# Optimization experiments

Measured on AMD Instinct MI355X. Metric: run time of the kernel, lower is better.

Reference implementation:

```python
import jax, jax.numpy as jnp
import numpy as np

IMG = 1024       # original image resolution implied by (1024 - 1) normalization
STRIDE = 16
TEMP = 0.1
EPS = 1e-12      # F.normalize eps


def setup_inputs() -> dict:
    key = jax.random.key(0)
    k1, k2, k3, k4, k5 = jax.random.split(key, 5)
    B, C, Hf, Wf, N = 32, 256, 64, 64, 128
    feats_src = jax.random.normal(k1, (B, C, Hf, Wf), dtype=jnp.float32)
    feats_trg = jax.random.normal(k2, (B, C, Hf, Wf), dtype=jnp.float32)
    kps_src = jax.random.uniform(k3, (B, N, 2), dtype=jnp.float32) * (IMG - 1)
    kps_trg = jax.random.uniform(k4, (B, N, 2), dtype=jnp.float32) * (IMG - 1)
    kps_mask = jax.random.randint(k5, (B, N), 0, 2, dtype=jnp.int32)
    return {"feats_src": feats_src, "feats_trg": feats_trg,
            "kps_src": kps_src, "kps_trg": kps_trg, "kps_mask": kps_mask}


def _l2norm_c(x):
    # F.normalize(x, dim=1): x / max(||x||_2, eps) along channel dim
    n = jnp.sqrt(jnp.sum(x * x, axis=1, keepdims=True))
    return x / jnp.maximum(n, EPS)


def _bilinear_sample(feats, kps):
    # feats: [B,C,Hf,Wf]; kps: [B,N,2] pixel coords in [0, IMG-1]
    # Equivalent to F.grid_sample(align_corners=True, bilinear) with
    # grid = kps/(IMG-1)*2-1 -> pixel coords kps/(IMG-1)*(size-1).
    B, C, Hf, Wf = feats.shape
    x = kps[..., 0] / (IMG - 1) * (Wf - 1)  # [B,N]
    y = kps[..., 1] / (IMG - 1) * (Hf - 1)
    x0 = jnp.clip(jnp.floor(x), 0, Wf - 1).astype(jnp.int32)
    y0 = jnp.clip(jnp.floor(y), 0, Hf - 1).astype(jnp.int32)
    x1 = jnp.clip(x0 + 1, 0, Wf - 1)
    y1 = jnp.clip(y0 + 1, 0, Hf - 1)
    fx = x - x0.astype(x.dtype)
    fy = y - y0.astype(y.dtype)
    ft = jnp.transpose(feats, (0, 2, 3, 1))      # [B,Hf,Wf,C]
    bb = jnp.arange(B)[:, None]                  # [B,1] broadcasts to [B,N]
    g = lambda yy, xx: ft[bb, yy, xx]            # [B,N,C]
    wa = ((1 - fx) * (1 - fy))[..., None]
    wb = ((1 - fx) * fy)[..., None]
    wc = (fx * (1 - fy))[..., None]
    wd = (fx * fy)[..., None]
    return wa * g(y0, x0) + wb * g(y1, x0) + wc * g(y0, x1) + wd * g(y1, x1)


def reference(feats_src, feats_trg, kps_src, kps_trg, kps_mask):
    B, C, Hf, Wf = feats_src.shape
    N = kps_src.shape[1]
    fs = _l2norm_c(feats_src)
    ftg = _l2norm_c(feats_trg)

    # Query features sampled at source keypoints: [B,N,C]
    q = _bilinear_sample(fs, kps_src)

    # Logits over all target spatial positions: [B,N,Hf*Wf]
    trg_flat = ftg.reshape(B, C, Hf * Wf)
    logits = jnp.einsum('bnc,bcm->bnm', q, trg_flat) / TEMP

    # Bilinear soft targets at target keypoints (feature-grid coords)
    gx = kps_trg[..., 0] / STRIDE
    gy = kps_trg[..., 1] / STRIDE
    x0 = jnp.clip(jnp.floor(gx), 0, Wf - 1).astype(jnp.int32)
    x1 = jnp.clip(x0 + 1, 0, Wf - 1)
    y0 = jnp.clip(jnp.floor(gy), 0, Hf - 1).astype(jnp.int32)
    y1 = jnp.clip(y0 + 1, 0, Hf - 1)
    x0f, x1f = x0.astype(gx.dtype), x1.astype(gx.dtype)
    y0f, y1f = y0.astype(gy.dtype), y1.astype(gy.dtype)
    wa = (x1f - gx) * (y1f - gy)
    wb = (x1f - gx) * (gy - y0f)
    wc = (gx - x0f) * (y1f - gy)
    wd = (gx - x0f) * (gy - y0f)

    m = (kps_mask != 0).astype(logits.dtype)     # [B,N]
    w = jnp.stack([wa, wb, wc, wd], axis=-1) * m[..., None]   # [B,N,4]
    idx = jnp.stack([y0 * Wf + x0, y1 * Wf + x0,
                     y0 * Wf + x1, y1 * Wf + x1], axis=-1)    # [B,N,4]
    bb = jnp.arange(B)[:, None, None]
    nn = jnp.arange(N)[None, :, None]
    soft_targets = jnp.zeros_like(logits).at[bb, nn, idx].add(w)

    log_probs = jax.nn.log_softmax(logits, axis=-1)
    loss = -(soft_targets * log_probs).sum(axis=-1)           # [B,N]
    denom = jnp.maximum(m.sum(), 1.0)
    return (loss * m).sum() / denom
```

## Files before the change

### kernel.cpp

```cpp
#include <hip/hip_runtime.h>
#include <math.h>

#define B_    32
#define C_    256
#define HF    64
#define WF    64
#define M_    4096
#define N_    128
#define IMGM1 1023.0f
#define TEMP_ 0.1f
#define EPS_  1e-12f
#define NCH   32
#define SAS   40

typedef __attribute__((ext_vector_type(8))) short short8;
typedef __attribute__((ext_vector_type(4))) float floatx4;

__device__ __forceinline__ unsigned short f2bf(float x) {
  unsigned int u = __float_as_uint(x);
  u += 0x7fffu + ((u >> 16) & 1u);
  return (unsigned short)(u >> 16);
}
__device__ __forceinline__ float bf2f(unsigned short h) {
  return __uint_as_float(((unsigned int)h) << 16);
}
__device__ __forceinline__ float wave_sum(float v) {
#pragma unroll
  for (int off = 32; off; off >>= 1) v += __shfl_down(v, off, 64);
  return v;
}

__device__ __forceinline__ void src_geom(float kx, float ky, int& x0, int& y0,
                                         int& x1, int& y1, float& fx, float& fy) {
  const float x = kx / IMGM1 * (float)(WF - 1);
  const float y = ky / IMGM1 * (float)(HF - 1);
  x0 = (int)fminf(fmaxf(floorf(x), 0.f), 63.f);
  y0 = (int)fminf(fmaxf(floorf(y), 0.f), 63.f);
  x1 = min(x0 + 1, 63);
  y1 = min(y0 + 1, 63);
  fx = x - (float)x0;
  fy = y - (float)y0;
}

__global__ __launch_bounds__(256) void k1a_stage(const float* __restrict__ fs,
                                                 const float* __restrict__ kps,
                                                 ushort* __restrict__ corner,
                                                 float* __restrict__ ssqg) {
  const int cg = blockIdx.x, b = blockIdx.y, t = threadIdx.x;
  const int c0 = cg * 2;
  __shared__ __align__(16) float plane[2 * M_];
  __shared__ float4 ssq2[256];

  const float4* src = (const float4*)(fs + ((size_t)(b * C_ + c0)) * M_);
  float4* dst = (float4*)plane;
#pragma unroll
  for (int i = 0; i < 8; i++) dst[t + 256 * i] = src[t + 256 * i];
  __syncthreads();

  const int n = t & 127, p = t >> 7;
  const int c = c0 + p;
  const float kx = kps[((size_t)b * N_ + n) * 2 + 0];
  const float ky = kps[((size_t)b * N_ + n) * 2 + 1];
  int x0, y0, x1, y1; float fx, fy;
  src_geom(kx, ky, x0, y0, x1, y1, fx, fy);

  const float* pl = plane + p * M_;
  const float f00 = pl[y0 * WF + x0];
  const float f10 = pl[y1 * WF + x0];
  const float f01 = pl[y0 * WF + x1];
  const float f11 = pl[y1 * WF + x1];

  ushort4 cr;
  cr.x = f2bf(f00); cr.y = f2bf(f10); cr.z = f2bf(f01); cr.w = f2bf(f11);
  *(ushort4*)&corner[(((size_t)b * C_ + c) * N_ + n) * 4] = cr;

  ssq2[t] = make_float4(f00 * f00, f10 * f10, f01 * f01, f11 * f11);
  __syncthreads();
  if (t < 128) {
    const float4 a = ssq2[t], bq = ssq2[t + 128];
    float* g = ssqg + ((size_t)b * N_ + t) * 4;
    atomicAdd(g + 0, a.x + bq.x);
    atomicAdd(g + 1, a.y + bq.y);
    atomicAdd(g + 2, a.z + bq.z);
    atomicAdd(g + 3, a.w + bq.w);
  }
}

__global__ __launch_bounds__(256) void k1b2_combine(const ushort* __restrict__ corner,
                                                    const float* __restrict__ ssqg,
                                                    const float* __restrict__ kps,
                                                    ushort* __restrict__ qbf) {
  const int cg = blockIdx.x, b = blockIdx.y, t = threadIdx.x;
  __shared__ float4 uw[128];
  __shared__ ushort sQ[32][137];

  if (t < 128) {
    const int n = t;
    const float kx = kps[((size_t)b * N_ + n) * 2 + 0];
    const float ky = kps[((size_t)b * N_ + n) * 2 + 1];
    int x0, y0, x1, y1; float fx, fy;
    src_geom(kx, ky, x0, y0, x1, y1, fx, fy);
    const float wa = (1.f - fx) * (1.f - fy), wb = (1.f - fx) * fy;
    const float wc = fx * (1.f - fy), wd = fx * fy;
    const float4 sq = *(const float4*)&ssqg[((size_t)b * N_ + n) * 4];
    const float r0 = 1.f / fmaxf(sqrtf(sq.x), EPS_);
    const float r1 = 1.f / fmaxf(sqrtf(sq.y), EPS_);
    const float r2 = 1.f / fmaxf(sqrtf(sq.z), EPS_);
    const float r3 = 1.f / fmaxf(sqrtf(sq.w), EPS_);
    uw[n] = make_float4(wa * r0, wb * r1, wc * r2, wd * r3);
  }
  __syncthreads();

  const ushort* cb = corner + (((size_t)b * C_ + cg * 32) * N_) * 4;
#pragma unroll
  for (int i = 0; i < 16; i++) {
    const int e = t + 256 * i;
    const int n = e & 127, cl = e >> 7;
    const ushort4 cr = *(const ushort4*)&cb[((size_t)cl * N_ + n) * 4];
    const float4 u = uw[n];
    const float qv = u.x * bf2f(cr.x) + u.y * bf2f(cr.y) +
                     u.z * bf2f(cr.z) + u.w * bf2f(cr.w);
    sQ[cl][n] = f2bf(qv);
  }
  __syncthreads();

  ushort* qb = qbf + (size_t)b * N_ * C_ + cg * 32;
#pragma unroll
  for (int i = 0; i < 4; i++) {
    const int o = t + 256 * i;
    const int n = o >> 3, c4 = (o & 7) * 4;
    ushort4 w4;
    w4.x = sQ[c4 + 0][n]; w4.y = sQ[c4 + 1][n];
    w4.z = sQ[c4 + 2][n]; w4.w = sQ[c4 + 3][n];
    *(ushort4*)&qb[(size_t)n * C_ + c4] = w4;
  }
}

__global__ __launch_bounds__(256, 4) void k2_mfma(const float* __restrict__ trg,
                                                  const ushort* __restrict__ qbf,
                                                  const float* __restrict__ kps_trg,
                                                  const int* __restrict__ mask,
                                                  float2* __restrict__ part,
                                                  float* __restrict__ tacc) {
  const int t = threadIdx.x;
  const int mb = blockIdx.x, b = blockIdx.y;
  const int m0 = mb * 128;
  const int wave = t >> 6, lane = t & 63;
  const int wn = wave >> 1, wm = wave & 1;
  const int lg = lane >> 4, ln = lane & 15;

  __shared__ __align__(16) short sA[128 * SAS];
  __shared__ __align__(16) short sB[128 * SAS];
  __shared__ __align__(16) float ssqp[16 * 128];
  __shared__ float scl[128];
  __shared__ float2 lser[128 * 2];
  __shared__ __align__(16) int   tidx[128][4];
  __shared__ __align__(16) float tw[128][4];
  __shared__ unsigned tmask[128];

  floatx4 acc[4][4];
#pragma unroll
  for (int i = 0; i < 4; i++)
#pragma unroll
    for (int j = 0; j < 4; j++) acc[i][j] = (floatx4)0.f;

  float ssq[8];
#pragma unroll
  for (int e = 0; e < 8; e++) ssq[e] = 0.f;

  const ushort* qb = qbf + (size_t)b * N_ * C_;
  const float*  tb = trg + (size_t)b * C_ * M_ + m0;
  const int kk  = 2 * (t >> 4);
  const int m4  = (t & 15) * 4;
  const int gB  = kk >> 3;
  const int kin = kk & 7;

  const ushort* qA0 = qb + (t >> 2) * C_ + (t & 3) * 8;
  const ushort* qA1 = qA0 + 64 * C_;
  const int aoff = (t >> 2) * SAS + (t & 3) * 8;
  const float* tbase = tb + (size_t)kk * M_ + m4;

  short8 rA0, rA1;
  float4 rBa0, rBa1, rBb0, rBb1;

  rA0 = *(const short8*)(qA0);
  rA1 = *(const short8*)(qA1);
  {
    const float* p0 = tbase;
    const float* p1 = p0 + M_;
    rBa0 = *(const float4*)p0;  rBa1 = *(const float4*)(p0 + 64);
    rBb0 = *(const float4*)p1;  rBb1 = *(const float4*)(p1 + 64);
  }

  for (int k0 = 0; k0 < C_; k0 += 32) {
    *(short8*)&sA[aoff] = rA0;
    *(short8*)&sA[aoff + 64 * SAS] = rA1;
    {
      const float v0[8] = {rBa0.x, rBa0.y, rBa0.z, rBa0.w, rBa1.x, rBa1.y, rBa1.z, rBa1.w};
      const float v1[8] = {rBb0.x, rBb0.y, rBb0.z, rBb0.w, rBb1.x, rBb1.y, rBb1.z, rBb1.w};
#pragma unroll
      for (int e = 0; e < 8; e++) {
        ssq[e] += v0[e] * v0[e] + v1[e] * v1[e];
        const int m = m4 + (e & 3) + ((e >> 2) << 6);
        const int fm = (m >> 3) & 3;
        const unsigned int pr = (unsigned int)f2bf(v0[e]) | ((unsigned int)f2bf(v1[e]) << 16);
        *(unsigned int*)&sB[m * SAS + ((gB ^ fm) << 3) + kin] = pr;
      }
    }
    {
      const int kn = k0 + 32;
      if (kn < C_) {
        rA0 = *(const short8*)(qA0 + kn);
        rA1 = *(const short8*)(qA1 + kn);
        const float* p0 = tbase + (size_t)kn * M_;
        const float* p1 = p0 + M_;
        rBa0 = *(const float4*)p0;  rBa1 = *(const float4*)(p0 + 64);
        rBb0 = *(const float4*)p1;  rBb1 = *(const float4*)(p1 + 64);
      }
    }
    __syncthreads();
    short8 af[4], bfr[4];
#pragma unroll
    for (int i = 0; i < 4; i++)
      af[i] = *(const short8*)&sA[(wn * 64 + i * 16 + ln) * SAS + (lg << 3)];
#pragma unroll
    for (int j = 0; j < 4; j++) {
      const int m = wm * 64 + j * 16 + ln;
      const int fm = (m >> 3) & 3;
      bfr[j] = *(const short8*)&sB[m * SAS + ((lg ^ fm) << 3)];
    }
#pragma unroll
    for (int i = 0; i < 4; i++)
#pragma unroll
      for (int j = 0; j < 4; j++)
        acc[i][j] = __builtin_amdgcn_mfma_f32_16x16x32_bf16(af[i], bfr[j], acc[i][j], 0, 0, 0);
    __syncthreads();
  }

  *(float4*)&ssqp[(t >> 4) * 128 + m4]      = make_float4(ssq[0], ssq[1], ssq[2], ssq[3]);
  *(float4*)&ssqp[(t >> 4) * 128 + m4 + 64] = make_float4(ssq[4], ssq[5], ssq[6], ssq[7]);
  __syncthreads();
  if (t < 128) {
    float s = 0.f;
#pragma unroll
    for (int g = 0; g < 16; g++) s += ssqp[g * 128 + t];
    scl[t] = 1.f / (fmaxf(sqrtf(s), EPS_) * TEMP_);
    const float kx = kps_trg[((size_t)b * N_ + t) * 2 + 0];
    const float ky = kps_trg[((size_t)b * N_ + t) * 2 + 1];
    const float gx = kx * (1.f / 16.f), gy = ky * (1.f / 16.f);
    const int x0 = (int)fminf(fmaxf(floorf(gx), 0.f), 63.f);
    const int y0 = (int)fminf(fmaxf(floorf(gy), 0.f), 63.f);
    const int x1 = min(x0 + 1, 63), y1 = min(y0 + 1, 63);
    const float x0f = (float)x0, x1f = (float)x1, y0f = (float)y0, y1f = (float)y1;
    const float mk = (mask[(size_t)b * N_ + t] != 0) ? 1.f : 0.f;
    const int i0 = y0 * WF + x0, i1 = y1 * WF + x0;
    const int i2 = y0 * WF + x1, i3 = y1 * WF + x1;
    const float w0 = (x1f - gx) * (y1f - gy) * mk;
    const float w1 = (x1f - gx) * (gy - y0f) * mk;
    const float w2 = (gx - x0f) * (y1f - gy) * mk;
    const float w3 = (gx - x0f) * (gy - y0f) * mk;
    tidx[t][0] = i0; tw[t][0] = w0;
    tidx[t][1] = i1; tw[t][1] = w1;
    tidx[t][2] = i2; tw[t][2] = w2;
    tidx[t][3] = i3; tw[t][3] = w3;
    unsigned tm = 0u;
    if (w0 != 0.f) tm |= 1u << (i0 >> 7);
    if (w1 != 0.f) tm |= 1u << (i1 >> 7);
    if (w2 != 0.f) tm |= 1u << (i2 >> 7);
    if (w3 != 0.f) tm |= 1u << (i3 >> 7);
    tmask[t] = tm;
  }
  __syncthreads();

  float scj[4];
#pragma unroll
  for (int j = 0; j < 4; j++) scj[j] = scl[wm * 64 + j * 16 + ln];
#pragma unroll
  for (int i = 0; i < 4; i++)
#pragma unroll
    for (int j = 0; j < 4; j++) acc[i][j] *= scj[j];

  const unsigned mbbit = 1u << mb;
#pragma unroll
  for (int i = 0; i < 4; i++) {
#pragma unroll
    for (int r = 0; r < 4; r++) {
      float mx = fmaxf(fmaxf(acc[i][0][r], acc[i][1][r]), fmaxf(acc[i][2][r], acc[i][3][r]));
#pragma unroll
      for (int msk = 1; msk < 16; msk <<= 1) mx = fmaxf(mx, __shfl_xor(mx, msk, 64));
      float sm = __expf(acc[i][0][r] - mx) + __expf(acc[i][1][r] - mx) +
                 __expf(acc[i][2][r] - mx) + __expf(acc[i][3][r] - mx);
#pragma unroll
      for (int msk = 1; msk < 16; msk <<= 1) sm += __shfl_xor(sm, msk, 64);
      if (ln == 0) lser[(wn * 64 + i * 16 + lg * 4 + r) * 2 + wm] = make_float2(mx, sm);

      const int n = wn * 64 + i * 16 + lg * 4 + r;
      if (tmask[n] & mbbit) {
        const int4  id4 = *(const int4*)&tidx[n][0];
        const float4 w4 = *(const float4*)&tw[n][0];
        const int   ida[4] = {id4.x, id4.y, id4.z, id4.w};
        const float wwa[4] = {w4.x, w4.y, w4.z, w4.w};
#pragma unroll
        for (int j = 0; j < 4; j++) {
          const int mg = m0 + wm * 64 + j * 16 + ln;
          const float lv = acc[i][j][r];
#pragma unroll
          for (int cc = 0; cc < 4; cc++)
            if (ida[cc] == mg && wwa[cc] != 0.f)
              atomicAdd(&tacc[(size_t)b * N_ + n], wwa[cc] * lv);
        }
      }
    }
  }
  __syncthreads();
  if (t < 128) {
    const float2 u = lser[t * 2 + 0], v = lser[t * 2 + 1];
    const float M = fmaxf(u.x, v.x);
    const float S = u.y * __expf(u.x - M) + v.y * __expf(v.x - M);
    part[((size_t)b * N_ + t) * NCH + mb] = make_float2(M, S);
  }
}

__global__ __launch_bounds__(128) void k4_comb(const float2* __restrict__ part,
                                               const float* __restrict__ tacc,
                                               const float* __restrict__ kps_trg,
                                               const int* __restrict__ mask,
                                               float* __restrict__ gs) {
  const int b = blockIdx.x, t = threadIdx.x;
  const float2* p = part + ((size_t)b * N_ + t) * NCH;
  float M = -INFINITY;
#pragma unroll 8
  for (int c = 0; c < NCH; c++) M = fmaxf(M, p[c].x);
  float S = 0.f;
#pragma unroll 8
  for (int c = 0; c < NCH; c++) S += p[c].y * __expf(p[c].x - M);
  const float lse = M + logf(S);

  const float kx = kps_trg[((size_t)b * N_ + t) * 2 + 0];
  const float ky = kps_trg[((size_t)b * N_ + t) * 2 + 1];
  const float gx = kx * (1.f / 16.f), gy = ky * (1.f / 16.f);
  const int x0 = (int)fminf(fmaxf(floorf(gx), 0.f), 63.f);
  const int y0 = (int)fminf(fmaxf(floorf(gy), 0.f), 63.f);
  const int x1 = min(x0 + 1, 63), y1 = min(y0 + 1, 63);
  const float mk = (mask[(size_t)b * N_ + t] != 0) ? 1.f : 0.f;
  const float wsum = (float)(x1 - x0) * (float)(y1 - y0) * mk;

  float loss = wsum * lse - tacc[(size_t)b * N_ + t];
  float cnt = mk;
  loss = wave_sum(loss);
  cnt = wave_sum(cnt);
  __shared__ float sl[2], sc2[2];
  if ((t & 63) == 0) { sl[t >> 6] = loss; sc2[t >> 6] = cnt; }
  __syncthreads();
  if (t == 0) {
    atomicAdd(&gs[0], sl[0] + sl[1]);
    atomicAdd(&gs[1], sc2[0] + sc2[1]);
  }
}

__global__ void k5_final(const float* __restrict__ gs, float* __restrict__ out) {
  out[0] = gs[0] / fmaxf(gs[1], 1.f);
}

extern "C" void kernel_launch(void* const* d_in, const int* in_sizes, int n_in,
                              void* d_out, int out_size, void* d_ws, size_t ws_size,
                              hipStream_t stream) {
  const float* feats_src = (const float*)d_in[0];
  const float* feats_trg = (const float*)d_in[1];
  const float* kps_src   = (const float*)d_in[2];
  const float* kps_trg   = (const float*)d_in[3];
  const int*   kps_mask  = (const int*)d_in[4];
  float* out = (float*)d_out;

  char* wsb = (char*)d_ws;
  float*  ssqg   = (float*)(wsb + 0);
  float*  tacc   = (float*)(wsb + 65536);
  float*  gs     = (float*)(wsb + 81920);
  ushort* corner = (ushort*)(wsb + 82432);
  ushort* qbf    = (ushort*)(wsb + 8471040);
  float2* part   = (float2*)(wsb + 10568192);

  hipMemsetAsync(wsb, 0, 81928, stream);

  k1a_stage<<<dim3(C_ / 2, B_), 256, 0, stream>>>(feats_src, kps_src, corner, ssqg);
  k1b2_combine<<<dim3(C_ / 32, B_), 256, 0, stream>>>(corner, ssqg, kps_src, qbf);
  k2_mfma<<<dim3(NCH, B_), 256, 0, stream>>>(feats_trg, qbf, kps_trg, kps_mask, part, tacc);
  k4_comb<<<dim3(B_), 128, 0, stream>>>(part, tacc, kps_trg, kps_mask, gs);
  k5_final<<<1, 1, 0, stream>>>(gs, out);
}
```

Before: 347.5 us.

## Shrink logits GEMM M-tile to 64 columns and transpose partial LSE layout

Halves the per-block M tile of the fused similarity/log-softmax kernel from 128 to 64, doubling the grid to 64 chunks per batch and shrinking per-thread accumulators and prefetch registers. The target-mask bitmap widens to 64 bits to match the new chunk count. The partial (max,sum) buffer is stored chunk-major so the combine kernel reads it coalesced across threads. More blocks and lower register use should raise occupancy and latency hiding, but the query tile is reloaded twice as often and the combine step reads twice as many partials.

```diff
diff --git a/kernel.cpp b/kernel.cpp
--- a/kernel.cpp
+++ b/kernel.cpp
@@ -10,7 +10,8 @@
 #define IMGM1 1023.0f
 #define TEMP_ 0.1f
 #define EPS_  1e-12f
-#define NCH   32
+#define NCH   64
+#define MT    64
 #define SAS   40
 
 typedef __attribute__((ext_vector_type(8))) short short8;
@@ -136,37 +137,35 @@
   }
 }
 
-__global__ __launch_bounds__(256, 4) void k2_mfma(const float* __restrict__ trg,
-                                                  const ushort* __restrict__ qbf,
-                                                  const float* __restrict__ kps_trg,
-                                                  const int* __restrict__ mask,
-                                                  float2* __restrict__ part,
-                                                  float* __restrict__ tacc) {
+__global__ __launch_bounds__(256) void k2_mfma(const float* __restrict__ trg,
+                                               const ushort* __restrict__ qbf,
+                                               const float* __restrict__ kps_trg,
+                                               const int* __restrict__ mask,
+                                               float2* __restrict__ part,
+                                               float* __restrict__ tacc) {
   const int t = threadIdx.x;
   const int mb = blockIdx.x, b = blockIdx.y;
-  const int m0 = mb * 128;
+  const int m0 = mb * MT;
   const int wave = t >> 6, lane = t & 63;
-  const int wn = wave >> 1, wm = wave & 1;
+  const int wn2 = wave >> 1, wm2 = wave & 1;
   const int lg = lane >> 4, ln = lane & 15;
 
   __shared__ __align__(16) short sA[128 * SAS];
-  __shared__ __align__(16) short sB[128 * SAS];
-  __shared__ __align__(16) float ssqp[16 * 128];
-  __shared__ float scl[128];
-  __shared__ float2 lser[128 * 2];
-  __shared__ __align__(16) int   tidx[128][4];
-  __shared__ __align__(16) float tw[128][4];
-  __shared__ unsigned tmask[128];
-
-  floatx4 acc[4][4];
+  __shared__ __align__(16) short sB[MT * SAS];
+  __shared__ __align__(16) float ssqp[16 * MT];
+  __shared__ float scl[MT];
+  __shared__ float2 lser[N_ * 2];
+  __shared__ __align__(16) int   tidx[N_][4];
+  __shared__ __align__(16) float tw[N_][4];
+  __shared__ unsigned long long tmask[N_];
+
+  floatx4 acc[4][2];
 #pragma unroll
   for (int i = 0; i < 4; i++)
 #pragma unroll
-    for (int j = 0; j < 4; j++) acc[i][j] = (floatx4)0.f;
-
-  float ssq[8];
-#pragma unroll
-  for (int e = 0; e < 8; e++) ssq[e] = 0.f;
+    for (int j = 0; j < 2; j++) acc[i][j] = (floatx4)0.f;
+
+  float ssq[4] = {0.f, 0.f, 0.f, 0.f};
 
   const ushort* qb = qbf + (size_t)b * N_ * C_;
   const float*  tb = trg + (size_t)b * C_ * M_ + m0;
@@ -181,27 +180,23 @@
   const float* tbase = tb + (size_t)kk * M_ + m4;
 
   short8 rA0, rA1;
-  float4 rBa0, rBa1, rBb0, rBb1;
+  float4 rB0, rB1;
 
   rA0 = *(const short8*)(qA0);
   rA1 = *(const short8*)(qA1);
-  {
-    const float* p0 = tbase;
-    const float* p1 = p0 + M_;
-    rBa0 = *(const float4*)p0;  rBa1 = *(const float4*)(p0 + 64);
-    rBb0 = *(const float4*)p1;  rBb1 = *(const float4*)(p1 + 64);
-  }
+  rB0 = *(const float4*)(tbase);
+  rB1 = *(const float4*)(tbase + M_);
 
   for (int k0 = 0; k0 < C_; k0 += 32) {
     *(short8*)&sA[aoff] = rA0;
     *(short8*)&sA[aoff + 64 * SAS] = rA1;
     {
-      const float v0[8] = {rBa0.x, rBa0.y, rBa0.z, rBa0.w, rBa1.x, rBa1.y, rBa1.z, rBa1.w};
-      const float v1[8] = {rBb0.x, rBb0.y, rBb0.z, rBb0.w, rBb1.x, rBb1.y, rBb1.z, rBb1.w};
-#pragma unroll
-      for (int e = 0; e < 8; e++) {
+      const float v0[4] = {rB0.x, rB0.y, rB0.z, rB0.w};
+      const float v1[4] = {rB1.x, rB1.y, rB1.z, rB1.w};
+#pragma unroll
+      for (int e = 0; e < 4; e++) {
         ssq[e] += v0[e] * v0[e] + v1[e] * v1[e];
-        const int m = m4 + (e & 3) + ((e >> 2) << 6);
+        const int m = m4 + e;
         const int fm = (m >> 3) & 3;
         const unsigned int pr = (unsigned int)f2bf(v0[e]) | ((unsigned int)f2bf(v1[e]) << 16);
         *(unsigned int*)&sB[m * SAS + ((gB ^ fm) << 3) + kin] = pr;
@@ -212,39 +207,38 @@
       if (kn < C_) {
         rA0 = *(const short8*)(qA0 + kn);
         rA1 = *(const short8*)(qA1 + kn);
-        const float* p0 = tbase + (size_t)kn * M_;
-        const float* p1 = p0 + M_;
-        rBa0 = *(const float4*)p0;  rBa1 = *(const float4*)(p0 + 64);
-        rBb0 = *(const float4*)p1;  rBb1 = *(const float4*)(p1 + 64);
+        rB0 = *(const float4*)(tbase + (size_t)kn * M_);
+        rB1 = *(const float4*)(tbase + (size_t)kn * M_ + M_);
       }
     }
     __syncthreads();
-    short8 af[4], bfr[4];
+    short8 af[4], bfr[2];
 #pragma unroll
     for (int i = 0; i < 4; i++)
-      af[i] = *(const short8*)&sA[(wn * 64 + i * 16 + ln) * SAS + (lg << 3)];
-#pragma unroll
-    for (int j = 0; j < 4; j++) {
-      const int m = wm * 64 + j * 16 + ln;
+      af[i] = *(const short8*)&sA[(wn2 * 64 + i * 16 + ln) * SAS + (lg << 3)];
+#pragma unroll
+    for (int j = 0; j < 2; j++) {
+      const int m = wm2 * 32 + j * 16 + ln;
       const int fm = (m >> 3) & 3;
       bfr[j] = *(const short8*)&sB[m * SAS + ((lg ^ fm) << 3)];
     }
 #pragma unroll
     for (int i = 0; i < 4; i++)
 #pragma unroll
-      for (int j = 0; j < 4; j++)
+      for (int j = 0; j < 2; j++)
         acc[i][j] = __builtin_amdgcn_mfma_f32_16x16x32_bf16(af[i], bfr[j], acc[i][j], 0, 0, 0);
     __syncthreads();
   }
 
-  *(float4*)&ssqp[(t >> 4) * 128 + m4]      = make_float4(ssq[0], ssq[1], ssq[2], ssq[3]);
-  *(float4*)&ssqp[(t >> 4) * 128 + m4 + 64] = make_float4(ssq[4], ssq[5], ssq[6], ssq[7]);
-  __syncthreads();
+  *(float4*)&ssqp[(t >> 4) * MT + m4] = make_float4(ssq[0], ssq[1], ssq[2], ssq[3]);
+  __syncthreads();
+  if (t < MT) {
+    float s = 0.f;
+#pragma unroll
+    for (int g = 0; g < 16; g++) s += ssqp[g * MT + t];
+    scl[t] = 1.f / (fmaxf(sqrtf(s), EPS_) * TEMP_);
+  }
   if (t < 128) {
-    float s = 0.f;
-#pragma unroll
-    for (int g = 0; g < 16; g++) s += ssqp[g * 128 + t];
-    scl[t] = 1.f / (fmaxf(sqrtf(s), EPS_) * TEMP_);
     const float kx = kps_trg[((size_t)b * N_ + t) * 2 + 0];
     const float ky = kps_trg[((size_t)b * N_ + t) * 2 + 1];
     const float gx = kx * (1.f / 16.f), gy = ky * (1.f / 16.f);
@@ -263,46 +257,45 @@
     tidx[t][1] = i1; tw[t][1] = w1;
     tidx[t][2] = i2; tw[t][2] = w2;
     tidx[t][3] = i3; tw[t][3] = w3;
-    unsigned tm = 0u;
-    if (w0 != 0.f) tm |= 1u << (i0 >> 7);
-    if (w1 != 0.f) tm |= 1u << (i1 >> 7);
-    if (w2 != 0.f) tm |= 1u << (i2 >> 7);
-    if (w3 != 0.f) tm |= 1u << (i3 >> 7);
+    unsigned long long tm = 0ull;
+    if (w0 != 0.f) tm |= 1ull << (i0 >> 6);
+    if (w1 != 0.f) tm |= 1ull << (i1 >> 6);
+    if (w2 != 0.f) tm |= 1ull << (i2 >> 6);
+    if (w3 != 0.f) tm |= 1ull << (i3 >> 6);
     tmask[t] = tm;
   }
   __syncthreads();
 
-  float scj[4];
-#pragma unroll
-  for (int j = 0; j < 4; j++) scj[j] = scl[wm * 64 + j * 16 + ln];
+  float scj[2];
+#pragma unroll
+  for (int j = 0; j < 2; j++) scj[j] = scl[wm2 * 32 + j * 16 + ln];
 #pragma unroll
   for (int i = 0; i < 4; i++)
 #pragma unroll
-    for (int j = 0; j < 4; j++) acc[i][j] *= scj[j];
-
-  const unsigned mbbit = 1u << mb;
+    for (int j = 0; j < 2; j++) acc[i][j] *= scj[j];
+
+  const unsigned long long mbbit = 1ull << mb;
 #pragma unroll
   for (int i = 0; i < 4; i++) {
 #pragma unroll
     for (int r = 0; r < 4; r++) {
-      float mx = fmaxf(fmaxf(acc[i][0][r], acc[i][1][r]), fmaxf(acc[i][2][r], acc[i][3][r]));
+      float mx = fmaxf(acc[i][0][r], acc[i][1][r]);
 #pragma unroll
       for (int msk = 1; msk < 16; msk <<= 1) mx = fmaxf(mx, __shfl_xor(mx, msk, 64));
-      float sm = __expf(acc[i][0][r] - mx) + __expf(acc[i][1][r] - mx) +
-                 __expf(acc[i][2][r] - mx) + __expf(acc[i][3][r] - mx);
+      float sm = __expf(acc[i][0][r] - mx) + __expf(acc[i][1][r] - mx);
 #pragma unroll
       for (int msk = 1; msk < 16; msk <<= 1) sm += __shfl_xor(sm, msk, 64);
-      if (ln == 0) lser[(wn * 64 + i * 16 + lg * 4 + r) * 2 + wm] = make_float2(mx, sm);
-
-      const int n = wn * 64 + i * 16 + lg * 4 + r;
+      const int n = wn2 * 64 + i * 16 + lg * 4 + r;
+      if (ln == 0) lser[n * 2 + wm2] = make_float2(mx, sm);
+
       if (tmask[n] & mbbit) {
         const int4  id4 = *(const int4*)&tidx[n][0];
         const float4 w4 = *(const float4*)&tw[n][0];
         const int   ida[4] = {id4.x, id4.y, id4.z, id4.w};
         const float wwa[4] = {w4.x, w4.y, w4.z, w4.w};
 #pragma unroll
-        for (int j = 0; j < 4; j++) {
-          const int mg = m0 + wm * 64 + j * 16 + ln;
+        for (int j = 0; j < 2; j++) {
+          const int mg = m0 + wm2 * 32 + j * 16 + ln;
           const float lv = acc[i][j][r];
 #pragma unroll
           for (int cc = 0; cc < 4; cc++)
@@ -317,7 +310,7 @@
     const float2 u = lser[t * 2 + 0], v = lser[t * 2 + 1];
     const float M = fmaxf(u.x, v.x);
     const float S = u.y * __expf(u.x - M) + v.y * __expf(v.x - M);
-    part[((size_t)b * N_ + t) * NCH + mb] = make_float2(M, S);
+    part[((size_t)b * NCH + mb) * N_ + t] = make_float2(M, S);
   }
 }
 
@@ -327,13 +320,16 @@
                                                const int* __restrict__ mask,
                                                float* __restrict__ gs) {
   const int b = blockIdx.x, t = threadIdx.x;
-  const float2* p = part + ((size_t)b * N_ + t) * NCH;
+  const float2* p = part + (size_t)b * NCH * N_ + t;
   float M = -INFINITY;
 #pragma unroll 8
-  for (int c = 0; c < NCH; c++) M = fmaxf(M, p[c].x);
+  for (int c = 0; c < NCH; c++) M = fmaxf(M, p[(size_t)c * N_].x);
   float S = 0.f;
 #pragma unroll 8
-  for (int c = 0; c < NCH; c++) S += p[c].y * __expf(p[c].x - M);
+  for (int c = 0; c < NCH; c++) {
+    const float2 v = p[(size_t)c * N_];
+    S += v.y * __expf(v.x - M);
+  }
   const float lse = M + logf(S);
 
   const float kx = kps_trg[((size_t)b * N_ + t) * 2 + 0];
```

New measurement: 337.9 us. 2.8% less time.
